# Optimization experiments

Measured on AMD Instinct MI355X. Metric: run time of the kernel, lower is better.

The kernel has to match this reference:

```python
import jax, jax.numpy as jnp
import numpy as np

BN_EPS = 1e-5

def _haar_details(x):
    # pywt.dwt2(x, 'haar') details for even H, W.
    # Block [[p, q], [r, s]] with p = x[2i,2j], q = x[2i,2j+1], r = x[2i+1,2j], s = x[2i+1,2j+1].
    # cH ('da'): detail along rows, approx along cols; cV ('ad'); cD ('dd').
    B, C, H, W = x.shape
    xb = x.reshape(B, C, H // 2, 2, W // 2, 2)
    p = xb[:, :, :, 0, :, 0]
    q = xb[:, :, :, 0, :, 1]
    r = xb[:, :, :, 1, :, 0]
    s = xb[:, :, :, 1, :, 1]
    cH = (p + q - r - s) * 0.5
    cV = (p - q + r - s) * 0.5
    cD = (p - q - r + s) * 0.5
    return cH, cV, cD

def setup_inputs() -> dict:
    key = jax.random.key(0)
    k1, k2 = jax.random.split(key)
    B, C, H, W = 8, 256, 128, 128
    x = jax.random.normal(k1, (B, C, H, W), dtype=jnp.float32)
    conv_w = jax.random.normal(k2, (C, 4 * C), dtype=jnp.float32) * (1.0 / np.sqrt(4 * C))
    gamma = jnp.ones((C,), dtype=jnp.float32)
    beta = jnp.zeros((C,), dtype=jnp.float32)
    return {"x": x, "conv_w": conv_w, "gamma": gamma, "beta": beta}

def reference(x, conv_w, gamma, beta):
    B, C, H, W = x.shape
    # Original detaches the wavelet branch (CPU numpy path) -> stop_gradient.
    xs = jax.lax.stop_gradient(x)
    cH, cV, cD = _haar_details(xs)
    # Bilinear upsample to (H, W); jax.image.resize bilinear == torch align_corners=False.
    up = lambda t: jax.image.resize(t, (B, C, H, W), method="bilinear")
    enhanced = jnp.concatenate([x, up(cH), up(cV), up(cD)], axis=1)  # [B, 4C, H, W]
    # 1x1 conv, no bias.
    y = jnp.einsum("bchw,oc->bohw", enhanced, conv_w)  # [B, C, H, W]
    # BatchNorm2d, training-mode (batch statistics, biased variance).
    mean = jnp.mean(y, axis=(0, 2, 3), keepdims=True)
    var = jnp.mean((y - mean) ** 2, axis=(0, 2, 3), keepdims=True)
    y_hat = (y - mean) * jax.lax.rsqrt(var + BN_EPS)
    out = jax.nn.relu(y_hat * gamma[None, :, None, None] + beta[None, :, None, None])
    return out
```

## Files before the change

kernel.cpp:

```cpp
#include <hip/hip_runtime.h>
#include <hip/hip_bf16.h>

typedef __bf16 bf16;
typedef __bf16 bf16x4 __attribute__((ext_vector_type(4)));
typedef __bf16 bf16x8 __attribute__((ext_vector_type(8)));
typedef float  f32x4  __attribute__((ext_vector_type(4)));

#define AS1 __attribute__((address_space(1)))
#define AS3 __attribute__((address_space(3)))

__device__ __forceinline__ void load16_to_lds(const bf16* g, bf16* l) {
    __builtin_amdgcn_global_load_lds((const AS1 unsigned int*)g,
                                     (AS3 unsigned int*)l, 16, 0, 0);
}

__global__ __launch_bounds__(256) void prep_w(const float* __restrict__ w,
                                              bf16* __restrict__ wb) {
    int idx = (blockIdx.x * 256 + threadIdx.x) * 4;
    const float4 v = *(const float4*)(w + idx);
    bf16x4 o; o[0]=(bf16)v.x; o[1]=(bf16)v.y; o[2]=(bf16)v.z; o[3]=(bf16)v.w;
    *(bf16x4*)(wb + idx) = o;
}

__global__ __launch_bounds__(256, 2) void fused_x(const float* __restrict__ x,
                                                  const bf16* __restrict__ W,
                                                  bf16* __restrict__ cT,
                                                  bf16* __restrict__ y1) {
    __shared__ bf16 tile[64 * 264];
    const int bid = blockIdx.x;
    const int wt = bid & 3, j = (bid >> 2) & 63, b = bid >> 8;
    const int t = threadIdx.x;
    const int w0 = wt * 32;

    for (int i = 0; i < 16; ++i) {
        int g = i * 256 + t;
        int c = g >> 4;
        int rem = g & 15;
        int dlt = rem >> 3, w4 = rem & 7;
        const float4 v = *(const float4*)(x +
            ((((size_t)b * 256 + c) * 128 + (2 * j + dlt)) * 128 + w0 + w4 * 4));
        int pos = dlt * 32 + w4 * 4;
        tile[(pos + 0) * 264 + c] = (bf16)v.x;
        tile[(pos + 1) * 264 + c] = (bf16)v.y;
        tile[(pos + 2) * 264 + c] = (bf16)v.z;
        tile[(pos + 3) * 264 + c] = (bf16)v.w;
    }
    __syncthreads();

    for (int i = 0; i < 2; ++i) {
        int q = i * 256 + t;
        int cq = q & 31, kc = q >> 5;
        bf16x8 vp = *(const bf16x8*)&tile[(2 * kc) * 264 + cq * 8];
        bf16x8 vq = *(const bf16x8*)&tile[(2 * kc + 1) * 264 + cq * 8];
        bf16x8 vr = *(const bf16x8*)&tile[(32 + 2 * kc) * 264 + cq * 8];
        bf16x8 vs = *(const bf16x8*)&tile[(33 + 2 * kc) * 264 + cq * 8];
        bf16x8 oh, ov, od;
        #pragma unroll
        for (int e = 0; e < 8; ++e) {
            float p = (float)vp[e], qq = (float)vq[e];
            float r = (float)vr[e], s = (float)vs[e];
            oh[e] = (bf16)(0.5f * (p + qq - r - s));
            ov[e] = (bf16)(0.5f * (p - qq + r - s));
            od[e] = (bf16)(0.5f * (p - qq - r + s));
        }
        size_t row = ((size_t)b * 4096 + j * 64 + wt * 16 + kc) * 768;
        *(bf16x8*)(cT + row + 0 * 256 + cq * 8) = oh;
        *(bf16x8*)(cT + row + 1 * 256 + cq * 8) = ov;
        *(bf16x8*)(cT + row + 2 * 256 + cq * 8) = od;
    }

    const int wave = t >> 6, lane = t & 63;
    const int quad = lane >> 4, l16 = lane & 15;
    const int wo = wave * 64;
    f32x4 acc[4][4] = {};
    for (int kk = 0; kk < 256; kk += 32) {
        bf16x8 xf[4], wf[4];
        #pragma unroll
        for (int i = 0; i < 4; ++i)
            xf[i] = *(const bf16x8*)&tile[(i * 16 + l16) * 264 + kk + quad * 8];
        #pragma unroll
        for (int jj = 0; jj < 4; ++jj)
            wf[jj] = *(const bf16x8*)(W +
                (size_t)(wo + jj * 16 + l16) * 1024 + kk + quad * 8);
        #pragma unroll
        for (int i = 0; i < 4; ++i)
            #pragma unroll
            for (int jj = 0; jj < 4; ++jj)
                acc[i][jj] = __builtin_amdgcn_mfma_f32_16x16x32_bf16(
                    xf[i], wf[jj], acc[i][jj], 0, 0, 0);
    }

    #pragma unroll
    for (int i = 0; i < 4; ++i) {
        int p = i * 16 + quad * 4;
        int h = 2 * j + (p >> 5), wc = w0 + (p & 31);
        #pragma unroll
        for (int jj = 0; jj < 4; ++jj) {
            int o = wo + jj * 16 + l16;
            bf16x4 v;
            #pragma unroll
            for (int r = 0; r < 4; ++r) v[r] = (bf16)acc[i][jj][r];
            *(bf16x4*)(y1 + ((size_t)b * 256 + o) * 16384 + h * 128 + wc) = v;
        }
    }
}

__global__ __launch_bounds__(256) void gemm2(const bf16* __restrict__ W,
                                             const bf16* __restrict__ cT,
                                             bf16* __restrict__ z) {
    __shared__ bf16 Xt[128 * 32];
    const int bid = blockIdx.x;
    const int m0 = (bid & 255) * 128, o0 = (bid >> 8) * 128;
    const int t = threadIdx.x;
    const int wave = t >> 6, lane = t & 63;
    const int quad = lane >> 4, l16 = lane & 15;
    const int wo = (wave >> 1) * 64, wm = (wave & 1) * 64;
    const int r_in = lane >> 2, cch = lane & 3;

    f32x4 acc[4][4] = {};
    const bf16* wbase = W + (size_t)o0 * 1024 + 256;
    const bf16* xbase = cT + (size_t)m0 * 768;

    for (int kk = 0; kk < 768; kk += 32) {
        {
            int row = wave * 32 + (lane >> 1);
        }
        #pragma unroll
        for (int i = 0; i < 2; ++i) {
            int rblk = wave * 2 + i;
            int row = rblk * 16 + r_in;
            load16_to_lds(xbase + (size_t)row * 768 + kk + cch * 8,
                          &Xt[rblk * 512 + lane * 8]);
        }
        __syncthreads();
        bf16x8 af[4], bfr[4];
        #pragma unroll
        for (int i = 0; i < 4; ++i)
            af[i] = *(const bf16x8*)(wbase +
                (size_t)(wo + i * 16 + l16) * 1024 + kk + quad * 8);
        #pragma unroll
        for (int jj = 0; jj < 4; ++jj)
            bfr[jj] = *(const bf16x8*)&Xt[(wm + jj * 16 + l16) * 32 + quad * 8];
        #pragma unroll
        for (int i = 0; i < 4; ++i)
            #pragma unroll
            for (int jj = 0; jj < 4; ++jj)
                acc[i][jj] = __builtin_amdgcn_mfma_f32_16x16x32_bf16(
                    bfr[jj], af[i], acc[i][jj], 0, 0, 0);
        __syncthreads();
    }

    #pragma unroll
    for (int i = 0; i < 4; ++i) {
        int o = o0 + wo + i * 16 + l16;
        #pragma unroll
        for (int jj = 0; jj < 4; ++jj) {
            int m = m0 + wm + jj * 16 + quad * 4;
            int bb = m >> 12, mp = m & 4095;
            bf16x4 v;
            #pragma unroll
            for (int r = 0; r < 4; ++r) v[r] = (bf16)acc[i][jj][r];
            *(bf16x4*)(z + ((size_t)bb * 256 + o) * 4096 + mp) = v;
        }
    }
}

__device__ __forceinline__ void load_zplane(const bf16* zp, float* zs, int t) {
    for (int i = 0; i < 2; ++i) {
        int idx = (i * 256 + t) * 8;
        int j = idx >> 6, k = idx & 63;
        bf16x8 v = *(const bf16x8*)(zp + idx);
        #pragma unroll
        for (int e = 0; e < 8; ++e) zs[j * 65 + k + e] = (float)v[e];
    }
}

__device__ __forceinline__ void up8(const float* zs, int base, float* u) {
    int h = base >> 7, w0 = base & 127;
    int j0 = h >> 1;
    int jn = (h & 1) ? min(j0 + 1, 63) : max(j0 - 1, 0);
    int K = w0 >> 1;
    float z0[6], z1[6];
    #pragma unroll
    for (int d = 0; d < 6; ++d) {
        int kc = min(max(K - 1 + d, 0), 63);
        z0[d] = zs[j0 * 65 + kc];
        z1[d] = zs[jn * 65 + kc];
    }
    #pragma unroll
    for (int e = 0; e < 8; ++e) {
        int a = (e >> 1) + 1;
        int bb = (e & 1) ? a + 1 : a - 1;
        u[e] = 0.5625f * z0[a] + 0.1875f * (z0[bb] + z1[a]) + 0.0625f * z1[bb];
    }
}

__global__ __launch_bounds__(256) void stats_k(const bf16* __restrict__ y1,
                                               const bf16* __restrict__ z,
                                               float* __restrict__ stats) {
    __shared__ float zs[64 * 65];
    __shared__ float red[8];
    const int bid = blockIdx.x;
    const int o = bid & 255, b = bid >> 8;
    const int t = threadIdx.x;
    const bf16* zp = z + ((size_t)b * 256 + o) * 4096;
    const bf16* yp = y1 + ((size_t)b * 256 + o) * 16384;
    load_zplane(zp, zs, t);
    __syncthreads();
    float s = 0.f, ss = 0.f;
    for (int i = 0; i < 8; ++i) {
        int base = (i * 256 + t) * 8;
        float u[8];
        up8(zs, base, u);
        bf16x8 yv = *(const bf16x8*)(yp + base);
        #pragma unroll
        for (int e = 0; e < 8; ++e) {
            float y = (float)yv[e] + u[e];
            s += y; ss += y * y;
        }
    }
    #pragma unroll
    for (int off = 32; off > 0; off >>= 1) {
        s += __shfl_down(s, off);
        ss += __shfl_down(ss, off);
    }
    if ((t & 63) == 0) { red[t >> 6] = s; red[4 + (t >> 6)] = ss; }
    __syncthreads();
    if (t == 0) {
        atomicAdd(&stats[o],       red[0] + red[1] + red[2] + red[3]);
        atomicAdd(&stats[256 + o], red[4] + red[5] + red[6] + red[7]);
    }
}

__global__ __launch_bounds__(256) void finalize_k(float* __restrict__ stats,
                                                  const float* __restrict__ gamma,
                                                  const float* __restrict__ beta) {
    int o = threadIdx.x;
    const float n = 131072.f;
    float mean = stats[o] / n;
    float var = stats[256 + o] / n - mean * mean;
    float rstd = rsqrtf(var + 1e-5f);
    float sc = rstd * gamma[o];
    stats[512 + o] = sc;
    stats[768 + o] = beta[o] - mean * sc;
}

__global__ __launch_bounds__(256) void apply_k(const bf16* __restrict__ y1,
                                               const bf16* __restrict__ z,
                                               const float* __restrict__ stats,
                                               float* __restrict__ out) {
    __shared__ float zs[64 * 65];
    const int bid = blockIdx.x;
    const int o = bid & 255, b = bid >> 8;
    const int t = threadIdx.x;
    const bf16* zp = z + ((size_t)b * 256 + o) * 4096;
    const bf16* yp = y1 + ((size_t)b * 256 + o) * 16384;
    float* op = out + ((size_t)b * 256 + o) * 16384;
    const float sc = stats[512 + o], sh = stats[768 + o];
    load_zplane(zp, zs, t);
    __syncthreads();
    for (int i = 0; i < 8; ++i) {
        int base = (i * 256 + t) * 8;
        float u[8];
        up8(zs, base, u);
        bf16x8 yv = *(const bf16x8*)(yp + base);
        float4 o0, o1;
        o0.x = fmaxf(fmaf((float)yv[0] + u[0], sc, sh), 0.f);
        o0.y = fmaxf(fmaf((float)yv[1] + u[1], sc, sh), 0.f);
        o0.z = fmaxf(fmaf((float)yv[2] + u[2], sc, sh), 0.f);
        o0.w = fmaxf(fmaf((float)yv[3] + u[3], sc, sh), 0.f);
        o1.x = fmaxf(fmaf((float)yv[4] + u[4], sc, sh), 0.f);
        o1.y = fmaxf(fmaf((float)yv[5] + u[5], sc, sh), 0.f);
        o1.z = fmaxf(fmaf((float)yv[6] + u[6], sc, sh), 0.f);
        o1.w = fmaxf(fmaf((float)yv[7] + u[7], sc, sh), 0.f);
        *(float4*)(op + base) = o0;
        *(float4*)(op + base + 4) = o1;
    }
}

extern "C" void kernel_launch(void* const* d_in, const int* in_sizes, int n_in,
                              void* d_out, int out_size, void* d_ws, size_t ws_size,
                              hipStream_t stream) {
    const float* x      = (const float*)d_in[0];
    const float* conv_w = (const float*)d_in[1];
    const float* gamma  = (const float*)d_in[2];
    const float* beta   = (const float*)d_in[3];
    float* out = (float*)d_out;

    char* ws = (char*)d_ws;
    bf16*  Wbf   = (bf16*)ws;
    bf16*  z     = (bf16*)(ws + (512ll << 10));
    float* stats = (float*)(ws + (512ll << 10) + (16ll << 20));
    bf16*  cT    = (bf16*)(ws + (512ll << 10) + (16ll << 20) + 4096);
    bf16*  y1    = (bf16*)(ws + (512ll << 10) + (64ll << 20) + 4096);

    hipMemsetAsync(stats, 0, 4096, stream);
    prep_w<<<256, 256, 0, stream>>>(conv_w, Wbf);
    fused_x<<<2048, 256, 0, stream>>>(x, Wbf, cT, y1);
    gemm2<<<512, 256, 0, stream>>>(Wbf, cT, z);
    stats_k<<<2048, 256, 0, stream>>>(y1, z, stats);
    finalize_k<<<1, 256, 0, stream>>>(stats, gamma, beta);
    apply_k<<<2048, 256, 0, stream>>>(y1, z, stats, out);
}
```

Baseline: 352.2 us.

## Prefetch weight fragments, swizzle LDS tile, batch x loads, raise occupancy bounds

Both GEMM kernels now software-pipeline the global weight-fragment loads one K-step ahead in registers, so MFMA work overlaps with the next weight fetch. In fused_x the 16 float4 loads of x are issued together before the LDS transpose writes, and the LDS tile gets an XOR swizzle on 8-element chunks to cut bank conflicts in the transposed writes and fragment reads. Launch bounds rise to 4 blocks per SM for both kernels, which adds latency hiding but limits registers per thread and may cause spills given the larger live register sets (v[16], prefetch buffers).

```diff
diff --git a/kernel.cpp b/kernel.cpp
--- a/kernel.cpp
+++ b/kernel.cpp
@@ -22,7 +22,11 @@
     *(bf16x4*)(wb + idx) = o;
 }
 
-__global__ __launch_bounds__(256, 2) void fused_x(const float* __restrict__ x,
+__device__ __forceinline__ int tix(int row, int chunk, int lo) {
+    return row * 264 + (((chunk ^ ((row >> 2) & 7)) << 3) | lo);
+}
+
+__global__ __launch_bounds__(256, 4) void fused_x(const float* __restrict__ x,
                                                   const bf16* __restrict__ W,
                                                   bf16* __restrict__ cT,
                                                   bf16* __restrict__ y1) {
@@ -31,29 +35,47 @@
     const int wt = bid & 3, j = (bid >> 2) & 63, b = bid >> 8;
     const int t = threadIdx.x;
     const int w0 = wt * 32;
-
+    const int wave = t >> 6, lane = t & 63;
+    const int quad = lane >> 4, l16 = lane & 15;
+    const int wo = wave * 64;
+
+    bf16x8 wf_cur[4], wf_nxt[4];
+    #pragma unroll
+    for (int jj = 0; jj < 4; ++jj)
+        wf_cur[jj] = *(const bf16x8*)(W +
+            (size_t)(wo + jj * 16 + l16) * 1024 + quad * 8);
+
+    float4 v[16];
+    #pragma unroll
     for (int i = 0; i < 16; ++i) {
         int g = i * 256 + t;
-        int c = g >> 4;
-        int rem = g & 15;
+        int c = g >> 4, rem = g & 15;
         int dlt = rem >> 3, w4 = rem & 7;
-        const float4 v = *(const float4*)(x +
+        v[i] = *(const float4*)(x +
             ((((size_t)b * 256 + c) * 128 + (2 * j + dlt)) * 128 + w0 + w4 * 4));
+    }
+    #pragma unroll
+    for (int i = 0; i < 16; ++i) {
+        int g = i * 256 + t;
+        int c = g >> 4, rem = g & 15;
+        int dlt = rem >> 3, w4 = rem & 7;
         int pos = dlt * 32 + w4 * 4;
-        tile[(pos + 0) * 264 + c] = (bf16)v.x;
-        tile[(pos + 1) * 264 + c] = (bf16)v.y;
-        tile[(pos + 2) * 264 + c] = (bf16)v.z;
-        tile[(pos + 3) * 264 + c] = (bf16)v.w;
+        int cs = tix(pos, c >> 3, c & 7) - pos * 264;
+        tile[(pos + 0) * 264 + cs] = (bf16)v[i].x;
+        tile[(pos + 1) * 264 + cs] = (bf16)v[i].y;
+        tile[(pos + 2) * 264 + cs] = (bf16)v[i].z;
+        tile[(pos + 3) * 264 + cs] = (bf16)v[i].w;
     }
     __syncthreads();
 
     for (int i = 0; i < 2; ++i) {
         int q = i * 256 + t;
         int cq = q & 31, kc = q >> 5;
-        bf16x8 vp = *(const bf16x8*)&tile[(2 * kc) * 264 + cq * 8];
-        bf16x8 vq = *(const bf16x8*)&tile[(2 * kc + 1) * 264 + cq * 8];
-        bf16x8 vr = *(const bf16x8*)&tile[(32 + 2 * kc) * 264 + cq * 8];
-        bf16x8 vs = *(const bf16x8*)&tile[(33 + 2 * kc) * 264 + cq * 8];
+        int r0 = 2 * kc, r1 = 2 * kc + 1, r2 = 32 + 2 * kc, r3 = 33 + 2 * kc;
+        bf16x8 vp = *(const bf16x8*)&tile[tix(r0, cq, 0)];
+        bf16x8 vq = *(const bf16x8*)&tile[tix(r1, cq, 0)];
+        bf16x8 vr = *(const bf16x8*)&tile[tix(r2, cq, 0)];
+        bf16x8 vs = *(const bf16x8*)&tile[tix(r3, cq, 0)];
         bf16x8 oh, ov, od;
         #pragma unroll
         for (int e = 0; e < 8; ++e) {
@@ -69,25 +91,28 @@
         *(bf16x8*)(cT + row + 2 * 256 + cq * 8) = od;
     }
 
-    const int wave = t >> 6, lane = t & 63;
-    const int quad = lane >> 4, l16 = lane & 15;
-    const int wo = wave * 64;
     f32x4 acc[4][4] = {};
+    #pragma unroll
     for (int kk = 0; kk < 256; kk += 32) {
-        bf16x8 xf[4], wf[4];
-        #pragma unroll
-        for (int i = 0; i < 4; ++i)
-            xf[i] = *(const bf16x8*)&tile[(i * 16 + l16) * 264 + kk + quad * 8];
-        #pragma unroll
-        for (int jj = 0; jj < 4; ++jj)
-            wf[jj] = *(const bf16x8*)(W +
-                (size_t)(wo + jj * 16 + l16) * 1024 + kk + quad * 8);
-        #pragma unroll
-        for (int i = 0; i < 4; ++i)
+        if (kk < 224) {
             #pragma unroll
             for (int jj = 0; jj < 4; ++jj)
-                acc[i][jj] = __builtin_amdgcn_mfma_f32_16x16x32_bf16(
-                    xf[i], wf[jj], acc[i][jj], 0, 0, 0);
+                wf_nxt[jj] = *(const bf16x8*)(W +
+                    (size_t)(wo + jj * 16 + l16) * 1024 + kk + 32 + quad * 8);
+        }
+        bf16x8 xf[4];
+        #pragma unroll
+        for (int i2 = 0; i2 < 4; ++i2)
+            xf[i2] = *(const bf16x8*)&tile[tix(i2 * 16 + l16,
+                                               (kk >> 3) + quad, 0)];
+        #pragma unroll
+        for (int i2 = 0; i2 < 4; ++i2)
+            #pragma unroll
+            for (int jj = 0; jj < 4; ++jj)
+                acc[i2][jj] = __builtin_amdgcn_mfma_f32_16x16x32_bf16(
+                    xf[i2], wf_cur[jj], acc[i2][jj], 0, 0, 0);
+        #pragma unroll
+        for (int jj = 0; jj < 4; ++jj) wf_cur[jj] = wf_nxt[jj];
     }
 
     #pragma unroll
@@ -97,17 +122,17 @@
         #pragma unroll
         for (int jj = 0; jj < 4; ++jj) {
             int o = wo + jj * 16 + l16;
-            bf16x4 v;
-            #pragma unroll
-            for (int r = 0; r < 4; ++r) v[r] = (bf16)acc[i][jj][r];
-            *(bf16x4*)(y1 + ((size_t)b * 256 + o) * 16384 + h * 128 + wc) = v;
-        }
-    }
-}
-
-__global__ __launch_bounds__(256) void gemm2(const bf16* __restrict__ W,
-                                             const bf16* __restrict__ cT,
-                                             bf16* __restrict__ z) {
+            bf16x4 vv;
+            #pragma unroll
+            for (int r = 0; r < 4; ++r) vv[r] = (bf16)acc[i][jj][r];
+            *(bf16x4*)(y1 + ((size_t)b * 256 + o) * 16384 + h * 128 + wc) = vv;
+        }
+    }
+}
+
+__global__ __launch_bounds__(256, 4) void gemm2(const bf16* __restrict__ W,
+                                                const bf16* __restrict__ cT,
+                                                bf16* __restrict__ z) {
     __shared__ bf16 Xt[128 * 32];
     const int bid = blockIdx.x;
     const int m0 = (bid & 255) * 128, o0 = (bid >> 8) * 128;
@@ -121,10 +146,14 @@
     const bf16* wbase = W + (size_t)o0 * 1024 + 256;
     const bf16* xbase = cT + (size_t)m0 * 768;
 
+    bf16x8 af_cur[4], af_nxt[4];
+    #pragma unroll
+    for (int i = 0; i < 4; ++i)
+        af_cur[i] = *(const bf16x8*)(wbase +
+            (size_t)(wo + i * 16 + l16) * 1024 + quad * 8);
+
+    #pragma unroll 2
     for (int kk = 0; kk < 768; kk += 32) {
-        {
-            int row = wave * 32 + (lane >> 1);
-        }
         #pragma unroll
         for (int i = 0; i < 2; ++i) {
             int rblk = wave * 2 + i;
@@ -133,11 +162,13 @@
                           &Xt[rblk * 512 + lane * 8]);
         }
         __syncthreads();
-        bf16x8 af[4], bfr[4];
-        #pragma unroll
-        for (int i = 0; i < 4; ++i)
-            af[i] = *(const bf16x8*)(wbase +
-                (size_t)(wo + i * 16 + l16) * 1024 + kk + quad * 8);
+        if (kk < 736) {
+            #pragma unroll
+            for (int i = 0; i < 4; ++i)
+                af_nxt[i] = *(const bf16x8*)(wbase +
+                    (size_t)(wo + i * 16 + l16) * 1024 + kk + 32 + quad * 8);
+        }
+        bf16x8 bfr[4];
         #pragma unroll
         for (int jj = 0; jj < 4; ++jj)
             bfr[jj] = *(const bf16x8*)&Xt[(wm + jj * 16 + l16) * 32 + quad * 8];
@@ -146,8 +177,10 @@
             #pragma unroll
             for (int jj = 0; jj < 4; ++jj)
                 acc[i][jj] = __builtin_amdgcn_mfma_f32_16x16x32_bf16(
-                    bfr[jj], af[i], acc[i][jj], 0, 0, 0);
+                    bfr[jj], af_cur[i], acc[i][jj], 0, 0, 0);
         __syncthreads();
+        #pragma unroll
+        for (int i = 0; i < 4; ++i) af_cur[i] = af_nxt[i];
     }
 
     #pragma unroll
@@ -157,10 +190,10 @@
         for (int jj = 0; jj < 4; ++jj) {
             int m = m0 + wm + jj * 16 + quad * 4;
             int bb = m >> 12, mp = m & 4095;
-            bf16x4 v;
-            #pragma unroll
-            for (int r = 0; r < 4; ++r) v[r] = (bf16)acc[i][jj][r];
-            *(bf16x4*)(z + ((size_t)bb * 256 + o) * 4096 + mp) = v;
+            bf16x4 vv;
+            #pragma unroll
+            for (int r = 0; r < 4; ++r) vv[r] = (bf16)acc[i][jj][r];
+            *(bf16x4*)(z + ((size_t)bb * 256 + o) * 4096 + mp) = vv;
         }
     }
 }
```

Measured after the change: 401.8 us. 14.1% more time.
